# Kernel tuning notes

Hardware: AMD Instinct MI355X
Metric: run time of the kernel (lower is better)

The kernel has to match this reference:

```python
import jax, jax.numpy as jnp
import numpy as np

N = 100000
E = 300000
D = 128
EPS = 1e-5


def sage_conv(x, edge_index, Wl, bl, Wr):
    # PyG SAGEConv: out = lin_l(mean_{j in N(i)} x_j) + lin_r(x_i)
    src, dst = edge_index[0], edge_index[1]
    n = x.shape[0]
    agg = jax.ops.segment_sum(x[src], dst, num_segments=n)            # [N, d]
    cnt = jax.ops.segment_sum(jnp.ones((src.shape[0],), x.dtype), dst, num_segments=n)
    mean = agg / jnp.maximum(cnt, 1.0)[:, None]
    return mean @ Wl.T + bl + x @ Wr.T


def setup_inputs() -> dict:
    key = jax.random.key(0)
    ks = jax.random.split(key, 16)
    s = 0.05
    inp = {
        "feat": jax.random.normal(ks[0], (N, D), jnp.float32),
        "e0": jax.random.randint(ks[1], (2, E), 0, N, jnp.int32),
        "e1": jax.random.randint(ks[2], (2, E), 0, N, jnp.int32),
        "e2": jax.random.randint(ks[3], (2, E), 0, N, jnp.int32),
    }
    # per-etype SAGEConv params (in=hidden=128)
    for i, k in zip(range(3), (ks[4], ks[5], ks[6])):
        ka, kb = jax.random.split(k)
        inp[f"Wl{i}"] = jax.random.normal(ka, (D, D), jnp.float32) * s
        inp[f"bl{i}"] = jnp.zeros((D,), jnp.float32)
        inp[f"Wr{i}"] = jax.random.normal(kb, (D, D), jnp.float32) * s
    ka, kb = jax.random.split(ks[7])
    inp["Wla"] = jax.random.normal(ka, (D, D), jnp.float32) * s
    inp["bla"] = jnp.zeros((D,), jnp.float32)
    inp["Wra"] = jax.random.normal(kb, (D, D), jnp.float32) * s
    ka, kb = jax.random.split(ks[8])
    inp["Wf"] = jax.random.normal(ka, (D, D), jnp.float32) * s
    inp["bf"] = jnp.zeros((D,), jnp.float32)
    inp["Wrf"] = jax.random.normal(kb, (D, D), jnp.float32) * s
    inp["gamma"] = jnp.ones((D,), jnp.float32)
    inp["beta"] = jnp.zeros((D,), jnp.float32)
    inp["wt"] = jnp.ones((3,), jnp.float32)
    return inp


def reference(feat, Wl0, bl0, Wr0, Wl1, bl1, Wr1, Wl2, bl2, Wr2,
              Wla, bla, Wra, Wf, bf, Wrf, gamma, beta, wt, e0, e1, e2):
    out0 = sage_conv(feat, e0, Wl0, bl0, Wr0)
    out1 = sage_conv(feat, e1, Wl1, bl1, Wr1)
    out2 = sage_conv(feat, e2, Wl2, bl2, Wr2)
    all_e = jnp.concatenate([e0, e1, e2], axis=1)   # [2, 3E]
    all_out = sage_conv(feat, all_e, Wla, bla, Wra)
    comb = wt[0] * out0 + wt[1] * out1 + wt[2] * out2 + all_out
    comb = jax.nn.relu(comb)
    # BatchNorm1d (training mode: batch stats over node dim, biased var)
    mu = jnp.mean(comb, axis=0)
    var = jnp.mean((comb - mu) ** 2, axis=0)
    comb = (comb - mu) * jax.lax.rsqrt(var + EPS) * gamma + beta
    # dropout p=0.0 -> identity
    return sage_conv(comb, all_e, Wf, bf, Wrf)
```

## Files before the change

kernel.cpp:

```cpp
#include <hip/hip_runtime.h>

#define NN 100000
#define NE 300000
#define DD 128
#define NBLKG 782
#define NBLKSEG 49

typedef short bf16x8 __attribute__((ext_vector_type(8)));
typedef float f32x4 __attribute__((ext_vector_type(4)));
typedef unsigned u32x4 __attribute__((ext_vector_type(4)));

__device__ __forceinline__ unsigned short f2b(float f) {
    union { float f; unsigned u; } c; c.f = f;
    unsigned u = c.u;
    return (unsigned short)((u + 0x7fffu + ((u >> 16) & 1u)) >> 16);
}
__device__ __forceinline__ float b2lo(unsigned u) {
    union { float f; unsigned u; } c; c.u = u << 16; return c.f;
}
__device__ __forceinline__ float b2hi(unsigned u) {
    union { float f; unsigned u; } c; c.u = u & 0xffff0000u; return c.f;
}
__device__ __forceinline__ unsigned pack2(float lo, float hi) {
    return (unsigned)f2b(lo) | ((unsigned)f2b(hi) << 16);
}

#define NB_FEAT 6250
#define NB_WT   449
#define NB_DEG  3516
__global__ __launch_bounds__(256) void prep_all(
    const float* __restrict__ feat, unsigned short* __restrict__ fb,
    const float* __restrict__ Wl0, const float* __restrict__ bl0, const float* __restrict__ Wr0,
    const float* __restrict__ Wl1, const float* __restrict__ bl1, const float* __restrict__ Wr1,
    const float* __restrict__ Wl2, const float* __restrict__ bl2, const float* __restrict__ Wr2,
    const float* __restrict__ Wla, const float* __restrict__ bla, const float* __restrict__ Wra,
    const float* __restrict__ Wf,  const float* __restrict__ bfv, const float* __restrict__ Wrf,
    const float* __restrict__ wt,
    unsigned short* __restrict__ WcatB, float* __restrict__ bias1,
    unsigned short* __restrict__ W2catB, float* __restrict__ bias2,
    const int* __restrict__ e0, const int* __restrict__ e1, const int* __restrict__ e2,
    int* __restrict__ deg) {
    int b = blockIdx.x, tid = threadIdx.x;
    if (b < NB_FEAT) {
        int gid = b * 256 + tid;
        if (gid >= NN * 16) return;
        const f32x4* f4 = (const f32x4*)feat;
        f32x4 a = __builtin_nontemporal_load(&f4[gid * 2]);
        f32x4 c = __builtin_nontemporal_load(&f4[gid * 2 + 1]);
        uint4 o;
        o.x = pack2(a.x, a.y); o.y = pack2(a.z, a.w);
        o.z = pack2(c.x, c.y); o.w = pack2(c.z, c.w);
        ((uint4*)fb)[gid] = o;
    } else if (b < NB_FEAT + NB_WT) {
        int idx = (b - NB_FEAT) * 256 + tid;
        float w0 = wt[0], w1 = wt[1], w2 = wt[2];
        if (idx < 81920) {
            int f = idx / 640, k = idx % 640;
            float v;
            if (k < 128)      v = w0 * Wl0[f * 128 + k];
            else if (k < 256) v = w1 * Wl1[f * 128 + (k - 128)];
            else if (k < 384) v = w2 * Wl2[f * 128 + (k - 256)];
            else if (k < 512) v = Wla[f * 128 + (k - 384)];
            else {
                int kk = k - 512;
                v = w0 * Wr0[f * 128 + kk] + w1 * Wr1[f * 128 + kk] +
                    w2 * Wr2[f * 128 + kk] + Wra[f * 128 + kk];
            }
            WcatB[idx] = f2b(v);
        } else if (idx < 81920 + 32768) {
            int j = idx - 81920;
            int f = j >> 8, k = j & 255;
            W2catB[j] = f2b((k < 128) ? Wf[f * 128 + k] : Wrf[f * 128 + (k - 128)]);
        } else if (idx < 81920 + 32768 + 128) {
            int f = idx - (81920 + 32768);
            bias1[f] = w0 * bl0[f] + w1 * bl1[f] + w2 * bl2[f] + bla[f];
            bias2[f] = bfv[f];
        }
    } else {
        int gid = (b - NB_FEAT - NB_WT) * 256 + tid;
        if (gid >= 3 * NE) return;
        int t = (gid < NE) ? 0 : ((gid < 2 * NE) ? 1 : 2);
        int i = gid - t * NE;
        const int* ep = (t == 0) ? e0 : ((t == 1) ? e1 : e2);
        atomicAdd(&deg[t * NN + ep[NE + i]], 1);
    }
}

__global__ __launch_bounds__(256) void scan_local(
    const int* __restrict__ deg, int* __restrict__ rsloc, int* __restrict__ bsum) {
    __shared__ int sc[256];
    int b = blockIdx.x, tid = threadIdx.x;
    int seg = b / NBLKSEG, blk = b % NBLKSEG;
    int g0 = seg * NN;
    int base = blk * 2048 + tid * 8;
    int vals[8]; int tsum = 0;
#pragma unroll
    for (int j = 0; j < 8; ++j) {
        int l = base + j;
        int d = (l < NN) ? deg[g0 + l] : 0;
        vals[j] = tsum; tsum += d;
    }
    sc[tid] = tsum;
    __syncthreads();
    for (int off = 1; off < 256; off <<= 1) {
        int v = (tid >= off) ? sc[tid - off] : 0;
        __syncthreads();
        sc[tid] += v;
        __syncthreads();
    }
    int excl = sc[tid] - tsum;
#pragma unroll
    for (int j = 0; j < 8; ++j) {
        int l = base + j;
        if (l < NN) rsloc[g0 + l] = excl + vals[j];
    }
    if (tid == 255) bsum[b] = sc[255];
}

__global__ void scan_bsum(int* __restrict__ bsum) {
    int tid = threadIdx.x;
    if (tid < 3) {
        int run = 0;
        for (int b = 0; b < NBLKSEG; ++b) {
            int idx = tid * NBLKSEG + b;
            int t = bsum[idx]; bsum[idx] = run; run += t;
        }
    }
}

__global__ __launch_bounds__(256) void scan_fix(
    const int* __restrict__ deg, const int* __restrict__ rsloc, const int* __restrict__ bsum,
    int* __restrict__ fillpos, int* __restrict__ rowstartU, int* __restrict__ degall) {
    int blk = blockIdx.x, tid = threadIdx.x;
    int base = blk * 2048 + tid * 8;
    int o0 = bsum[blk], o1 = bsum[NBLKSEG + blk], o2 = bsum[2 * NBLKSEG + blk];
#pragma unroll
    for (int j = 0; j < 8; ++j) {
        int l = base + j;
        if (l < NN) {
            int d0 = deg[l], d1 = deg[NN + l], d2 = deg[2 * NN + l];
            int rU = (rsloc[l] + o0) + (rsloc[NN + l] + o1) + (rsloc[2 * NN + l] + o2);
            fillpos[l] = rU;
            fillpos[NN + l] = rU + d0;
            fillpos[2 * NN + l] = rU + d0 + d1;
            rowstartU[l] = rU;
            degall[l] = d0 + d1 + d2;
        }
    }
}

__global__ __launch_bounds__(256) void fill_csr(
    const int* __restrict__ e0, const int* __restrict__ e1, const int* __restrict__ e2,
    int* __restrict__ fillpos, int* __restrict__ csrU) {
    int gid = blockIdx.x * 256 + threadIdx.x;
    if (gid >= 3 * NE) return;
    int t = (gid < NE) ? 0 : ((gid < 2 * NE) ? 1 : 2);
    int i = gid - t * NE;
    const int* ep = (t == 0) ? e0 : ((t == 1) ? e1 : e2);
    int src = ep[i], dst = ep[NE + i];
    int p = atomicAdd(&fillpos[t * NN + dst], 1);
    csrU[p] = src;
}

__global__ __launch_bounds__(256) void gather1(
    const unsigned short* __restrict__ featB,
    const int* __restrict__ deg, const int* __restrict__ rowstartU,
    const int* __restrict__ degall, const int* __restrict__ csrU,
    unsigned short* __restrict__ meanB) {
    int n = __builtin_amdgcn_readfirstlane((int)((blockIdx.x * 256 + threadIdx.x) >> 6));
    if (n >= NN) return;
    int lane = threadIdx.x & 63;
    int d0 = deg[n], d1 = deg[NN + n];
    int dall = degall[n];
    int b1 = d0, b2 = d0 + d1;
    const int* cp = csrU + rowstartU[n];

    unsigned f0 = *((const unsigned*)(featB + (size_t)cp[0] * DD) + lane);
    unsigned f1 = *((const unsigned*)(featB + (size_t)cp[1] * DD) + lane);
    unsigned f2 = *((const unsigned*)(featB + (size_t)cp[2] * DD) + lane);
    unsigned f3 = *((const unsigned*)(featB + (size_t)cp[3] * DD) + lane);
    int i4 = cp[4], i5 = cp[5];
    float p0 = 0.f, p1 = 0.f;
    float sA0 = 0.f, sA1 = 0.f, sB0 = 0.f, sB1 = 0.f;
    for (int j = 0; j < dall; ++j) {
        if (j == b1) { sA0 = p0; sA1 = p1; }
        if (j == b2) { sB0 = p0; sB1 = p1; }
        unsigned u = f0;
        f0 = f1; f1 = f2; f2 = f3;
        f3 = *((const unsigned*)(featB + (size_t)i4 * DD) + lane);
        i4 = i5;
        i5 = cp[j + 6];
        p0 += b2lo(u); p1 += b2hi(u);
    }
    if (b2 == dall) { sB0 = p0; sB1 = p1; }
    if (b1 == dall) { sA0 = p0; sA1 = p1; }

    int d2 = dall - b2;
    float inv0 = 1.0f / fmaxf((float)d0, 1.0f);
    float inv1 = 1.0f / fmaxf((float)d1, 1.0f);
    float inv2 = 1.0f / fmaxf((float)d2, 1.0f);
    float m10 = sB0 - sA0, m11 = sB1 - sA1;
    float m20 = p0 - sB0,  m21 = p1 - sB1;
    unsigned* outp = (unsigned*)(meanB + (size_t)n * 384) + lane;
    __builtin_nontemporal_store(pack2(sA0 * inv0, sA1 * inv0), outp);
    __builtin_nontemporal_store(pack2(m10 * inv1, m11 * inv1), outp + 64);
    __builtin_nontemporal_store(pack2(m20 * inv2, m21 * inv2), outp + 128);
}

__global__ __launch_bounds__(256) void gemm1_tile(
    const unsigned short* __restrict__ meanB, const unsigned short* __restrict__ featB,
    const int* __restrict__ deg, const int* __restrict__ degall,
    const unsigned short* __restrict__ WcatB, const float* __restrict__ bias1,
    unsigned short* __restrict__ comb, float* __restrict__ partials) {
    __shared__ unsigned short ABs[65536 / 2];
    unsigned short* As = ABs;
    unsigned short* Bs = ABs + 16384;
    int tid = threadIdx.x;
    int wid = tid >> 6, lane = tid & 63;
    int quad = lane >> 4, m16 = lane & 15;
    int nb = blockIdx.x * 128;
    int mb = (wid & 1) * 64, fb = (wid >> 1) * 64;
    f32x4 acc[4][4];
#pragma unroll
    for (int mi = 0; mi < 4; ++mi)
#pragma unroll
        for (int fi = 0; fi < 4; ++fi) acc[mi][fi] = (f32x4){0.f, 0.f, 0.f, 0.f};

    for (int kc = 0; kc < 5; ++kc) {
        __syncthreads();
#pragma unroll
        for (int it = 0; it < 8; ++it) {
            int idx = it * 256 + tid;
            int row = idx >> 4, chunk = idx & 15;
            int s = chunk >> 2, q = chunk & 3;
            int gr = min(nb + row, NN - 1);
            u32x4 v;
            if (kc < 3) {
                v = *(const u32x4*)(meanB + (size_t)gr * 384 + kc * 128 + chunk * 8);
            } else if (kc == 3) {
                u32x4 m0 = *(const u32x4*)(meanB + (size_t)gr * 384 + chunk * 8);
                u32x4 m1 = *(const u32x4*)(meanB + (size_t)gr * 384 + 128 + chunk * 8);
                u32x4 m2 = *(const u32x4*)(meanB + (size_t)gr * 384 + 256 + chunk * 8);
                int dd0 = deg[gr], dd1 = deg[NN + gr], dal = degall[gr];
                float inva = 1.0f / fmaxf((float)dal, 1.0f);
                float w0 = (float)dd0 * inva;
                float w1 = (float)dd1 * inva;
                float w2 = (float)(dal - dd0 - dd1) * inva;
                v.x = pack2(w0 * b2lo(m0.x) + w1 * b2lo(m1.x) + w2 * b2lo(m2.x),
                            w0 * b2hi(m0.x) + w1 * b2hi(m1.x) + w2 * b2hi(m2.x));
                v.y = pack2(w0 * b2lo(m0.y) + w1 * b2lo(m1.y) + w2 * b2lo(m2.y),
                            w0 * b2hi(m0.y) + w1 * b2hi(m1.y) + w2 * b2hi(m2.y));
                v.z = pack2(w0 * b2lo(m0.z) + w1 * b2lo(m1.z) + w2 * b2lo(m2.z),
                            w0 * b2hi(m0.z) + w1 * b2hi(m1.z) + w2 * b2hi(m2.z));
                v.w = pack2(w0 * b2lo(m0.w) + w1 * b2lo(m1.w) + w2 * b2lo(m2.w),
                            w0 * b2hi(m0.w) + w1 * b2hi(m1.w) + w2 * b2hi(m2.w));
            } else {
                v = *(const u32x4*)(featB + (size_t)gr * DD + chunk * 8);
            }
            *(u32x4*)&As[(((s * 128 + row) * 4) + q) * 8] = v;
        }
#pragma unroll
        for (int it = 0; it < 8; ++it) {
            int idx = it * 256 + tid;
            int f = idx >> 4, chunk = idx & 15;
            int s = chunk >> 2, q = chunk & 3;
            u32x4 v = *(const u32x4*)(WcatB + (size_t)f * 640 + kc * 128 + chunk * 8);
            *(u32x4*)&Bs[(((s * 128 + f) * 4) + q) * 8] = v;
        }
        __syncthreads();
#pragma unroll
        for (int s = 0; s < 4; ++s) {
            bf16x8 av[4], bv[4];
#pragma unroll
            for (int mi = 0; mi < 4; ++mi)
                av[mi] = *(const bf16x8*)&As[(((s * 128 + mb + mi * 16 + m16) * 4) + quad) * 8];
#pragma unroll
            for (int fi = 0; fi < 4; ++fi)
                bv[fi] = *(const bf16x8*)&Bs[(((s * 128 + fb + fi * 16 + m16) * 4) + quad) * 8];
#pragma unroll
            for (int mi = 0; mi < 4; ++mi)
#pragma unroll
                for (int fi = 0; fi < 4; ++fi)
                    acc[mi][fi] = __builtin_amdgcn_mfma_f32_16x16x32_bf16(av[mi], bv[fi], acc[mi][fi], 0, 0, 0);
        }
    }
    __syncthreads();
    float* bnS = (float*)ABs;
    float* bnQ = bnS + 128;
    if (tid < 128) { bnS[tid] = 0.f; bnQ[tid] = 0.f; }
    __syncthreads();
#pragma unroll
    for (int fi = 0; fi < 4; ++fi) {
        int f = fb + fi * 16 + m16;
        float bb = bias1[f];
        float s = 0.f, q = 0.f;
#pragma unroll
        for (int mi = 0; mi < 4; ++mi) {
#pragma unroll
            for (int r = 0; r < 4; ++r) {
                int row = nb + mb + mi * 16 + quad * 4 + r;
                float v = fmaxf(acc[mi][fi][r] + bb, 0.f);
                if (row < NN) {
                    s += v; q += v * v;
                    comb[(size_t)row * DD + f] = f2b(v);
                }
            }
        }
        atomicAdd(&bnS[f], s);
        atomicAdd(&bnQ[f], q);
    }
    __syncthreads();
    if (tid < 128) {
        partials[(size_t)tid * NBLKG + blockIdx.x] = bnS[tid];
        partials[(size_t)(128 + tid) * NBLKG + blockIdx.x] = bnQ[tid];
    }
}

__global__ __launch_bounds__(256) void bnfin(
    const float* __restrict__ partials,
    const float* __restrict__ gamma, const float* __restrict__ beta,
    float* __restrict__ bnA, float* __restrict__ bnB) {
    __shared__ float rs[256], rq[256];
    int f = blockIdx.x, tid = threadIdx.x;
    float s = 0.f, q = 0.f;
    for (int r = tid; r < NBLKG; r += 256) {
        s += partials[(size_t)f * NBLKG + r];
        q += partials[(size_t)(128 + f) * NBLKG + r];
    }
    rs[tid] = s; rq[tid] = q;
    __syncthreads();
    for (int off = 128; off > 0; off >>= 1) {
        if (tid < off) { rs[tid] += rs[tid + off]; rq[tid] += rq[tid + off]; }
        __syncthreads();
    }
    if (tid == 0) {
        float mu = rs[0] / (float)NN;
        float var = fmaxf(rq[0] / (float)NN - mu * mu, 0.f);
        float a = gamma[f] * rsqrtf(var + 1e-5f);
        bnA[f] = a;
        bnB[f] = beta[f] - mu * a;
    }
}

__global__ __launch_bounds__(256) void gather2(
    const unsigned short* __restrict__ comb,
    const int* __restrict__ rowstartU, const int* __restrict__ degall,
    const int* __restrict__ csrU,
    const float* __restrict__ bnA, const float* __restrict__ bnB,
    unsigned short* __restrict__ meanC) {
    int n = __builtin_amdgcn_readfirstlane((int)((blockIdx.x * 256 + threadIdx.x) >> 6));
    if (n >= NN) return;
    int lane = threadIdx.x & 63;
    int dall = degall[n];
    const int* cp = csrU + rowstartU[n];

    unsigned f0 = *((const unsigned*)(comb + (size_t)cp[0] * DD) + lane);
    unsigned f1 = *((const unsigned*)(comb + (size_t)cp[1] * DD) + lane);
    unsigned f2 = *((const unsigned*)(comb + (size_t)cp[2] * DD) + lane);
    unsigned f3 = *((const unsigned*)(comb + (size_t)cp[3] * DD) + lane);
    int i4 = cp[4], i5 = cp[5];
    float p0 = 0.f, p1 = 0.f;
    for (int j = 0; j < dall; ++j) {
        unsigned u = f0;
        f0 = f1; f1 = f2; f2 = f3;
        f3 = *((const unsigned*)(comb + (size_t)i4 * DD) + lane);
        i4 = i5;
        i5 = cp[j + 6];
        p0 += b2lo(u); p1 += b2hi(u);
    }

    float v0 = 0.f, v1 = 0.f;
    if (dall > 0) {
        float inv = 1.0f / (float)dall;
        float2 a = *(const float2*)&bnA[lane * 2];
        float2 b = *(const float2*)&bnB[lane * 2];
        v0 = a.x * (p0 * inv) + b.x;
        v1 = a.y * (p1 * inv) + b.y;
    }
    __builtin_nontemporal_store(pack2(v0, v1),
                                (unsigned*)(meanC + (size_t)n * DD) + lane);
}

__global__ __launch_bounds__(256) void gemm2_tile(
    const unsigned short* __restrict__ meanC, const unsigned short* __restrict__ comb,
    const float* __restrict__ bnA, const float* __restrict__ bnB,
    const unsigned short* __restrict__ W2catB, const float* __restrict__ bias2,
    float* __restrict__ out) {
    __shared__ unsigned short ABs[65536 / 2];
    unsigned short* As = ABs;
    unsigned short* Bs = ABs + 16384;
    int tid = threadIdx.x;
    int wid = tid >> 6, lane = tid & 63;
    int quad = lane >> 4, m16 = lane & 15;
    int nb = blockIdx.x * 128;
    int mb = (wid & 1) * 64, fb = (wid >> 1) * 64;
    f32x4 acc[4][4];
#pragma unroll
    for (int mi = 0; mi < 4; ++mi)
#pragma unroll
        for (int fi = 0; fi < 4; ++fi) acc[mi][fi] = (f32x4){0.f, 0.f, 0.f, 0.f};

    for (int kc = 0; kc < 2; ++kc) {
        __syncthreads();
#pragma unroll
        for (int it = 0; it < 8; ++it) {
            int idx = it * 256 + tid;
            int row = idx >> 4, chunk = idx & 15;
            int s = chunk >> 2, q = chunk & 3;
            int gr = min(nb + row, NN - 1);
            u32x4 v;
            if (kc == 0) {
                v = *(const u32x4*)(meanC + (size_t)gr * DD + chunk * 8);
            } else {
                u32x4 c4 = *(const u32x4*)(comb + (size_t)gr * DD + chunk * 8);
                int cb = chunk * 8;
                float4 a0 = *(const float4*)&bnA[cb], a1 = *(const float4*)&bnA[cb + 4];
                float4 b0 = *(const float4*)&bnB[cb], b1 = *(const float4*)&bnB[cb + 4];
                v.x = pack2(a0.x * b2lo(c4.x) + b0.x, a0.y * b2hi(c4.x) + b0.y);
                v.y = pack2(a0.z * b2lo(c4.y) + b0.z, a0.w * b2hi(c4.y) + b0.w);
                v.z = pack2(a1.x * b2lo(c4.z) + b1.x, a1.y * b2hi(c4.z) + b1.y);
                v.w = pack2(a1.z * b2lo(c4.w) + b1.z, a1.w * b2hi(c4.w) + b1.w);
            }
            *(u32x4*)&As[(((s * 128 + row) * 4) + q) * 8] = v;
        }
#pragma unroll
        for (int it = 0; it < 8; ++it) {
            int idx = it * 256 + tid;
            int f = idx >> 4, chunk = idx & 15;
            int s = chunk >> 2, q = chunk & 3;
            u32x4 v = *(const u32x4*)(W2catB + (size_t)f * 256 + kc * 128 + chunk * 8);
            *(u32x4*)&Bs[(((s * 128 + f) * 4) + q) * 8] = v;
        }
        __syncthreads();
#pragma unroll
        for (int s = 0; s < 4; ++s) {
            bf16x8 av[4], bv[4];
#pragma unroll
            for (int mi = 0; mi < 4; ++mi)
                av[mi] = *(const bf16x8*)&As[(((s * 128 + mb + mi * 16 + m16) * 4) + quad) * 8];
#pragma unroll
            for (int fi = 0; fi < 4; ++fi)
                bv[fi] = *(const bf16x8*)&Bs[(((s * 128 + fb + fi * 16 + m16) * 4) + quad) * 8];
#pragma unroll
            for (int mi = 0; mi < 4; ++mi)
#pragma unroll
                for (int fi = 0; fi < 4; ++fi)
                    acc[mi][fi] = __builtin_amdgcn_mfma_f32_16x16x32_bf16(av[mi], bv[fi], acc[mi][fi], 0, 0, 0);
        }
    }
#pragma unroll
    for (int fi = 0; fi < 4; ++fi) {
        int f = fb + fi * 16 + m16;
        float bb = bias2[f];
#pragma unroll
        for (int mi = 0; mi < 4; ++mi) {
#pragma unroll
            for (int r = 0; r < 4; ++r) {
                int row = nb + mb + mi * 16 + quad * 4 + r;
                if (row < NN)
                    __builtin_nontemporal_store(acc[mi][fi][r] + bb,
                                                &out[(size_t)row * DD + f]);
            }
        }
    }
}

extern "C" void kernel_launch(void* const* d_in, const int* in_sizes, int n_in,
                              void* d_out, int out_size, void* d_ws, size_t ws_size,
                              hipStream_t stream) {
    const float* feat = (const float*)d_in[0];
    const int* e0 = (const int*)d_in[1];
    const int* e1 = (const int*)d_in[2];
    const int* e2 = (const int*)d_in[3];
    const float* Wl0 = (const float*)d_in[4];
    const float* bl0 = (const float*)d_in[5];
    const float* Wr0 = (const float*)d_in[6];
    const float* Wl1 = (const float*)d_in[7];
    const float* bl1 = (const float*)d_in[8];
    const float* Wr1 = (const float*)d_in[9];
    const float* Wl2 = (const float*)d_in[10];
    const float* bl2 = (const float*)d_in[11];
    const float* Wr2 = (const float*)d_in[12];
    const float* Wla = (const float*)d_in[13];
    const float* bla = (const float*)d_in[14];
    const float* Wra = (const float*)d_in[15];
    const float* Wf  = (const float*)d_in[16];
    const float* bfv = (const float*)d_in[17];
    const float* Wrf = (const float*)d_in[18];
    const float* gamma = (const float*)d_in[19];
    const float* beta  = (const float*)d_in[20];
    const float* wt    = (const float*)d_in[21];

    int* deg      = (int*)d_ws;
    int* rsloc    = deg + 3 * NN;
    int* fillpos  = rsloc + 3 * NN;
    int* csrU     = fillpos + 3 * NN;
    int* bsum     = csrU + 3 * NE + 8;
    int* rowstartU = bsum + 160;
    int* degall    = rowstartU + NN;
    float* partials = (float*)(degall + NN);
    float* bias1  = partials + 256 * NBLKG;
    float* bias2  = bias1 + 128;
    float* bnA    = bias2 + 128;
    float* bnB    = bnA + 128;
    unsigned short* WcatB  = (unsigned short*)(bnB + 128);
    unsigned short* W2catB = WcatB + 81920;
    unsigned short* comb   = W2catB + 32768;
    unsigned short* featB  = comb + (size_t)NN * DD;
    unsigned short* meanB  = featB + (size_t)NN * DD;
    unsigned short* meanC  = meanB + (size_t)NN * 384;

    hipMemsetAsync(deg, 0, (size_t)3 * NN * sizeof(int), stream);
    hipMemsetAsync(csrU + 3 * NE, 0, 8 * sizeof(int), stream);

    prep_all<<<NB_FEAT + NB_WT + NB_DEG, 256, 0, stream>>>(
        feat, featB,
        Wl0, bl0, Wr0, Wl1, bl1, Wr1, Wl2, bl2, Wr2,
        Wla, bla, Wra, Wf, bfv, Wrf, wt,
        WcatB, bias1, W2catB, bias2,
        e0, e1, e2, deg);
    scan_local<<<147, 256, 0, stream>>>(deg, rsloc, bsum);
    scan_bsum<<<1, 64, 0, stream>>>(bsum);
    scan_fix<<<NBLKSEG, 256, 0, stream>>>(deg, rsloc, bsum, fillpos, rowstartU, degall);
    fill_csr<<<3516, 256, 0, stream>>>(e0, e1, e2, fillpos, csrU);

    gather1<<<25000, 256, 0, stream>>>(featB, deg, rowstartU, degall, csrU, meanB);
    gemm1_tile<<<NBLKG, 256, 0, stream>>>(meanB, featB, deg, degall, WcatB, bias1,
                                          comb, partials);
    bnfin<<<128, 256, 0, stream>>>(partials, gamma, beta, bnA, bnB);
    gather2<<<25000, 256, 0, stream>>>(comb, rowstartU, degall, csrU, bnA, bnB, meanC);
    gemm2_tile<<<NBLKG, 256, 0, stream>>>(meanC, comb, bnA, bnB, W2catB, bias2,
                                          (float*)d_out);
}
```

Before: 523.8 us.

## Load GEMM operands directly from global memory and precompute all-edge mean in gather

Both GEMM kernels drop their LDS staging and barriers, and each wave loads its MFMA A and B fragments straight from global memory. gather1 now also writes the all-edge mean as a fourth 128-column slice, so gemm1 no longer recombines the three per-type means with degree weights. Removing LDS use may raise occupancy and cuts sync overhead. In exchange, global loads become strided and uncoalesced per wave, and each weight row is fetched redundantly by every wave; gather1 also writes an extra 128 columns per node.

```diff
diff --git a/kernel.cpp b/kernel.cpp
--- a/kernel.cpp
+++ b/kernel.cpp
@@ -159,7 +159,7 @@
     const int* ep = (t == 0) ? e0 : ((t == 1) ? e1 : e2);
     int src = ep[i], dst = ep[NE + i];
     int p = atomicAdd(&fillpos[t * NN + dst], 1);
-    csrU[p] = src;
+    csrU[t == 0 ? p : p] = src;
 }
 
 __global__ __launch_bounds__(256) void gather1(
@@ -199,22 +199,21 @@
     float inv0 = 1.0f / fmaxf((float)d0, 1.0f);
     float inv1 = 1.0f / fmaxf((float)d1, 1.0f);
     float inv2 = 1.0f / fmaxf((float)d2, 1.0f);
+    float inva = 1.0f / fmaxf((float)dall, 1.0f);
     float m10 = sB0 - sA0, m11 = sB1 - sA1;
     float m20 = p0 - sB0,  m21 = p1 - sB1;
-    unsigned* outp = (unsigned*)(meanB + (size_t)n * 384) + lane;
+    unsigned* outp = (unsigned*)(meanB + (size_t)n * 512) + lane;
     __builtin_nontemporal_store(pack2(sA0 * inv0, sA1 * inv0), outp);
     __builtin_nontemporal_store(pack2(m10 * inv1, m11 * inv1), outp + 64);
     __builtin_nontemporal_store(pack2(m20 * inv2, m21 * inv2), outp + 128);
+    __builtin_nontemporal_store(pack2(p0 * inva,  p1 * inva),  outp + 192);
 }
 
 __global__ __launch_bounds__(256) void gemm1_tile(
     const unsigned short* __restrict__ meanB, const unsigned short* __restrict__ featB,
-    const int* __restrict__ deg, const int* __restrict__ degall,
     const unsigned short* __restrict__ WcatB, const float* __restrict__ bias1,
     unsigned short* __restrict__ comb, float* __restrict__ partials) {
-    __shared__ unsigned short ABs[65536 / 2];
-    unsigned short* As = ABs;
-    unsigned short* Bs = ABs + 16384;
+    __shared__ float bnP[256];
     int tid = threadIdx.x;
     int wid = tid >> 6, lane = tid & 63;
     int quad = lane >> 4, m16 = lane & 15;
@@ -226,57 +225,33 @@
 #pragma unroll
         for (int fi = 0; fi < 4; ++fi) acc[mi][fi] = (f32x4){0.f, 0.f, 0.f, 0.f};
 
+    const unsigned short* aP[4];
+    const unsigned short* fP[4];
+    const unsigned short* bP[4];
+#pragma unroll
+    for (int mi = 0; mi < 4; ++mi) {
+        int r = min(nb + mb + mi * 16 + m16, NN - 1);
+        aP[mi] = meanB + (size_t)r * 512;
+        fP[mi] = featB + (size_t)r * DD;
+    }
+#pragma unroll
+    for (int fi = 0; fi < 4; ++fi)
+        bP[fi] = WcatB + (size_t)(fb + fi * 16 + m16) * 640;
+
+    int ko = quad * 8;
+#pragma unroll
     for (int kc = 0; kc < 5; ++kc) {
-        __syncthreads();
-#pragma unroll
-        for (int it = 0; it < 8; ++it) {
-            int idx = it * 256 + tid;
-            int row = idx >> 4, chunk = idx & 15;
-            int s = chunk >> 2, q = chunk & 3;
-            int gr = min(nb + row, NN - 1);
-            u32x4 v;
-            if (kc < 3) {
-                v = *(const u32x4*)(meanB + (size_t)gr * 384 + kc * 128 + chunk * 8);
-            } else if (kc == 3) {
-                u32x4 m0 = *(const u32x4*)(meanB + (size_t)gr * 384 + chunk * 8);
-                u32x4 m1 = *(const u32x4*)(meanB + (size_t)gr * 384 + 128 + chunk * 8);
-                u32x4 m2 = *(const u32x4*)(meanB + (size_t)gr * 384 + 256 + chunk * 8);
-                int dd0 = deg[gr], dd1 = deg[NN + gr], dal = degall[gr];
-                float inva = 1.0f / fmaxf((float)dal, 1.0f);
-                float w0 = (float)dd0 * inva;
-                float w1 = (float)dd1 * inva;
-                float w2 = (float)(dal - dd0 - dd1) * inva;
-                v.x = pack2(w0 * b2lo(m0.x) + w1 * b2lo(m1.x) + w2 * b2lo(m2.x),
-                            w0 * b2hi(m0.x) + w1 * b2hi(m1.x) + w2 * b2hi(m2.x));
-                v.y = pack2(w0 * b2lo(m0.y) + w1 * b2lo(m1.y) + w2 * b2lo(m2.y),
-                            w0 * b2hi(m0.y) + w1 * b2hi(m1.y) + w2 * b2hi(m2.y));
-                v.z = pack2(w0 * b2lo(m0.z) + w1 * b2lo(m1.z) + w2 * b2lo(m2.z),
-                            w0 * b2hi(m0.z) + w1 * b2hi(m1.z) + w2 * b2hi(m2.z));
-                v.w = pack2(w0 * b2lo(m0.w) + w1 * b2lo(m1.w) + w2 * b2lo(m2.w),
-                            w0 * b2hi(m0.w) + w1 * b2hi(m1.w) + w2 * b2hi(m2.w));
-            } else {
-                v = *(const u32x4*)(featB + (size_t)gr * DD + chunk * 8);
-            }
-            *(u32x4*)&As[(((s * 128 + row) * 4) + q) * 8] = v;
-        }
-#pragma unroll
-        for (int it = 0; it < 8; ++it) {
-            int idx = it * 256 + tid;
-            int f = idx >> 4, chunk = idx & 15;
-            int s = chunk >> 2, q = chunk & 3;
-            u32x4 v = *(const u32x4*)(WcatB + (size_t)f * 640 + kc * 128 + chunk * 8);
-            *(u32x4*)&Bs[(((s * 128 + f) * 4) + q) * 8] = v;
-        }
-        __syncthreads();
 #pragma unroll
         for (int s = 0; s < 4; ++s) {
+            int k = s * 32 + ko;
             bf16x8 av[4], bv[4];
 #pragma unroll
             for (int mi = 0; mi < 4; ++mi)
-                av[mi] = *(const bf16x8*)&As[(((s * 128 + mb + mi * 16 + m16) * 4) + quad) * 8];
+                av[mi] = (kc < 4) ? *(const bf16x8*)(aP[mi] + kc * 128 + k)
+                                  : *(const bf16x8*)(fP[mi] + k);
 #pragma unroll
             for (int fi = 0; fi < 4; ++fi)
-                bv[fi] = *(const bf16x8*)&Bs[(((s * 128 + fb + fi * 16 + m16) * 4) + quad) * 8];
+                bv[fi] = *(const bf16x8*)(bP[fi] + kc * 128 + k);
 #pragma unroll
             for (int mi = 0; mi < 4; ++mi)
 #pragma unroll
@@ -284,9 +259,9 @@
                     acc[mi][fi] = __builtin_amdgcn_mfma_f32_16x16x32_bf16(av[mi], bv[fi], acc[mi][fi], 0, 0, 0);
         }
     }
-    __syncthreads();
-    float* bnS = (float*)ABs;
-    float* bnQ = bnS + 128;
+
+    float* bnS = bnP;
+    float* bnQ = bnP + 128;
     if (tid < 128) { bnS[tid] = 0.f; bnQ[tid] = 0.f; }
     __syncthreads();
 #pragma unroll
@@ -386,9 +361,6 @@
     const float* __restrict__ bnA, const float* __restrict__ bnB,
     const unsigned short* __restrict__ W2catB, const float* __restrict__ bias2,
     float* __restrict__ out) {
-    __shared__ unsigned short ABs[65536 / 2];
-    unsigned short* As = ABs;
-    unsigned short* Bs = ABs + 16384;
     int tid = threadIdx.x;
     int wid = tid >> 6, lane = tid & 63;
     int quad = lane >> 4, m16 = lane & 15;
@@ -400,54 +372,59 @@
 #pragma unroll
         for (int fi = 0; fi < 4; ++fi) acc[mi][fi] = (f32x4){0.f, 0.f, 0.f, 0.f};
 
-    for (int kc = 0; kc < 2; ++kc) {
-        __syncthreads();
-#pragma unroll
-        for (int it = 0; it < 8; ++it) {
-            int idx = it * 256 + tid;
-            int row = idx >> 4, chunk = idx & 15;
-            int s = chunk >> 2, q = chunk & 3;
-            int gr = min(nb + row, NN - 1);
-            u32x4 v;
-            if (kc == 0) {
-                v = *(const u32x4*)(meanC + (size_t)gr * DD + chunk * 8);
-            } else {
-                u32x4 c4 = *(const u32x4*)(comb + (size_t)gr * DD + chunk * 8);
-                int cb = chunk * 8;
-                float4 a0 = *(const float4*)&bnA[cb], a1 = *(const float4*)&bnA[cb + 4];
-                float4 b0 = *(const float4*)&bnB[cb], b1 = *(const float4*)&bnB[cb + 4];
-                v.x = pack2(a0.x * b2lo(c4.x) + b0.x, a0.y * b2hi(c4.x) + b0.y);
-                v.y = pack2(a0.z * b2lo(c4.y) + b0.z, a0.w * b2hi(c4.y) + b0.w);
-                v.z = pack2(a1.x * b2lo(c4.z) + b1.x, a1.y * b2hi(c4.z) + b1.y);
-                v.w = pack2(a1.z * b2lo(c4.w) + b1.z, a1.w * b2hi(c4.w) + b1.w);
-            }
-            *(u32x4*)&As[(((s * 128 + row) * 4) + q) * 8] = v;
-        }
-#pragma unroll
-        for (int it = 0; it < 8; ++it) {
-            int idx = it * 256 + tid;
-            int f = idx >> 4, chunk = idx & 15;
-            int s = chunk >> 2, q = chunk & 3;
-            u32x4 v = *(const u32x4*)(W2catB + (size_t)f * 256 + kc * 128 + chunk * 8);
-            *(u32x4*)&Bs[(((s * 128 + f) * 4) + q) * 8] = v;
-        }
-        __syncthreads();
-#pragma unroll
-        for (int s = 0; s < 4; ++s) {
-            bf16x8 av[4], bv[4];
-#pragma unroll
-            for (int mi = 0; mi < 4; ++mi)
-                av[mi] = *(const bf16x8*)&As[(((s * 128 + mb + mi * 16 + m16) * 4) + quad) * 8];
+    const unsigned short* mP[4];
+    const unsigned short* cP[4];
+    const unsigned short* bP[4];
+#pragma unroll
+    for (int mi = 0; mi < 4; ++mi) {
+        int r = min(nb + mb + mi * 16 + m16, NN - 1);
+        mP[mi] = meanC + (size_t)r * DD;
+        cP[mi] = comb + (size_t)r * DD;
+    }
+#pragma unroll
+    for (int fi = 0; fi < 4; ++fi)
+        bP[fi] = W2catB + (size_t)(fb + fi * 16 + m16) * 256;
+
+    int ko = quad * 8;
+#pragma unroll
+    for (int s = 0; s < 4; ++s) {
+        int k = s * 32 + ko;
+        bf16x8 av[4], bv[4];
+#pragma unroll
+        for (int mi = 0; mi < 4; ++mi) av[mi] = *(const bf16x8*)(mP[mi] + k);
+#pragma unroll
+        for (int fi = 0; fi < 4; ++fi) bv[fi] = *(const bf16x8*)(bP[fi] + k);
+#pragma unroll
+        for (int mi = 0; mi < 4; ++mi)
 #pragma unroll
             for (int fi = 0; fi < 4; ++fi)
-                bv[fi] = *(const bf16x8*)&Bs[(((s * 128 + fb + fi * 16 + m16) * 4) + quad) * 8];
-#pragma unroll
-            for (int mi = 0; mi < 4; ++mi)
-#pragma unroll
-                for (int fi = 0; fi < 4; ++fi)
-                    acc[mi][fi] = __builtin_amdgcn_mfma_f32_16x16x32_bf16(av[mi], bv[fi], acc[mi][fi], 0, 0, 0);
-        }
-    }
+                acc[mi][fi] = __builtin_amdgcn_mfma_f32_16x16x32_bf16(av[mi], bv[fi], acc[mi][fi], 0, 0, 0);
+    }
+#pragma unroll
+    for (int s = 0; s < 4; ++s) {
+        int k = s * 32 + ko;
+        float4 a0 = *(const float4*)&bnA[k], a1 = *(const float4*)&bnA[k + 4];
+        float4 b0 = *(const float4*)&bnB[k], b1 = *(const float4*)&bnB[k + 4];
+        bf16x8 av[4], bv[4];
+#pragma unroll
+        for (int mi = 0; mi < 4; ++mi) {
+            u32x4 c4 = *(const u32x4*)(cP[mi] + k);
+            u32x4 rv;
+            rv.x = pack2(a0.x * b2lo(c4.x) + b0.x, a0.y * b2hi(c4.x) + b0.y);
+            rv.y = pack2(a0.z * b2lo(c4.y) + b0.z, a0.w * b2hi(c4.y) + b0.w);
+            rv.z = pack2(a1.x * b2lo(c4.z) + b1.x, a1.y * b2hi(c4.z) + b1.y);
+            rv.w = pack2(a1.z * b2lo(c4.w) + b1.z, a1.w * b2hi(c4.w) + b1.w);
+            av[mi] = *(const bf16x8*)&rv;
+        }
+#pragma unroll
+        for (int fi = 0; fi < 4; ++fi) bv[fi] = *(const bf16x8*)(bP[fi] + 128 + k);
+#pragma unroll
+        for (int mi = 0; mi < 4; ++mi)
+#pragma unroll
+            for (int fi = 0; fi < 4; ++fi)
+                acc[mi][fi] = __builtin_amdgcn_mfma_f32_16x16x32_bf16(av[mi], bv[fi], acc[mi][fi], 0, 0, 0);
+    }
+
 #pragma unroll
     for (int fi = 0; fi < 4; ++fi) {
         int f = fb + fi * 16 + m16;
@@ -508,7 +485,7 @@
     unsigned short* comb   = W2catB + 32768;
     unsigned short* featB  = comb + (size_t)NN * DD;
     unsigned short* meanB  = featB + (size_t)NN * DD;
-    unsigned short* meanC  = meanB + (size_t)NN * 384;
+    unsigned short* meanC  = meanB + (size_t)NN * 512;
 
     hipMemsetAsync(deg, 0, (size_t)3 * NN * sizeof(int), stream);
     hipMemsetAsync(csrU + 3 * NE, 0, 8 * sizeof(int), stream);
@@ -525,8 +502,7 @@
     fill_csr<<<3516, 256, 0, stream>>>(e0, e1, e2, fillpos, csrU);
 
     gather1<<<25000, 256, 0, stream>>>(featB, deg, rowstartU, degall, csrU, meanB);
-    gemm1_tile<<<NBLKG, 256, 0, stream>>>(meanB, featB, deg, degall, WcatB, bias1,
-                                          comb, partials);
+    gemm1_tile<<<NBLKG, 256, 0, stream>>>(meanB, featB, WcatB, bias1, comb, partials);
     bnfin<<<128, 256, 0, stream>>>(partials, gamma, beta, bnA, bnB);
     gather2<<<25000, 256, 0, stream>>>(comb, rowstartU, degall, csrU, bnA, bnB, meanC);
     gemm2_tile<<<NBLKG, 256, 0, stream>>>(meanC, comb, bnA, bnB, W2catB, bias2,
```

Result: slower. 578.5 us (+10.4%).

## Write all-edge mean in gather, read weights directly from global in GEMMs

Applied to the files above, without the earlier changes.

gather1 now also writes the all-edge mean as a fourth 128-wide segment, so the meanB row stride grows from 384 to 512. This lets gemm1 skip rebuilding that mean from the three per-type means and degrees. Both GEMM kernels stop staging the weight tile in LDS and load B fragments straight from global/L2 through per-lane pointers. The A tile uses an XOR-swizzled row-major LDS layout with nontemporal loads. The trade is extra gather write traffic and uncached-style global weight loads inside the MFMA loop, against halved LDS use and less staging work.

```diff
diff --git a/kernel.cpp b/kernel.cpp
--- a/kernel.cpp
+++ b/kernel.cpp
@@ -199,22 +199,21 @@
     float inv0 = 1.0f / fmaxf((float)d0, 1.0f);
     float inv1 = 1.0f / fmaxf((float)d1, 1.0f);
     float inv2 = 1.0f / fmaxf((float)d2, 1.0f);
+    float inva = 1.0f / fmaxf((float)dall, 1.0f);
     float m10 = sB0 - sA0, m11 = sB1 - sA1;
     float m20 = p0 - sB0,  m21 = p1 - sB1;
-    unsigned* outp = (unsigned*)(meanB + (size_t)n * 384) + lane;
+    unsigned* outp = (unsigned*)(meanB + (size_t)n * 512) + lane;
     __builtin_nontemporal_store(pack2(sA0 * inv0, sA1 * inv0), outp);
     __builtin_nontemporal_store(pack2(m10 * inv1, m11 * inv1), outp + 64);
     __builtin_nontemporal_store(pack2(m20 * inv2, m21 * inv2), outp + 128);
+    __builtin_nontemporal_store(pack2(p0 * inva,  p1 * inva),  outp + 192);
 }
 
 __global__ __launch_bounds__(256) void gemm1_tile(
     const unsigned short* __restrict__ meanB, const unsigned short* __restrict__ featB,
-    const int* __restrict__ deg, const int* __restrict__ degall,
     const unsigned short* __restrict__ WcatB, const float* __restrict__ bias1,
     unsigned short* __restrict__ comb, float* __restrict__ partials) {
-    __shared__ unsigned short ABs[65536 / 2];
-    unsigned short* As = ABs;
-    unsigned short* Bs = ABs + 16384;
+    __shared__ unsigned short As[128 * 128];
     int tid = threadIdx.x;
     int wid = tid >> 6, lane = tid & 63;
     int quad = lane >> 4, m16 = lane & 15;
@@ -226,57 +225,36 @@
 #pragma unroll
         for (int fi = 0; fi < 4; ++fi) acc[mi][fi] = (f32x4){0.f, 0.f, 0.f, 0.f};
 
+    const unsigned short* bP[4];
+#pragma unroll
+    for (int fi = 0; fi < 4; ++fi)
+        bP[fi] = WcatB + (size_t)(fb + fi * 16 + m16) * 640;
+
     for (int kc = 0; kc < 5; ++kc) {
         __syncthreads();
 #pragma unroll
         for (int it = 0; it < 8; ++it) {
             int idx = it * 256 + tid;
             int row = idx >> 4, chunk = idx & 15;
-            int s = chunk >> 2, q = chunk & 3;
             int gr = min(nb + row, NN - 1);
-            u32x4 v;
-            if (kc < 3) {
-                v = *(const u32x4*)(meanB + (size_t)gr * 384 + kc * 128 + chunk * 8);
-            } else if (kc == 3) {
-                u32x4 m0 = *(const u32x4*)(meanB + (size_t)gr * 384 + chunk * 8);
-                u32x4 m1 = *(const u32x4*)(meanB + (size_t)gr * 384 + 128 + chunk * 8);
-                u32x4 m2 = *(const u32x4*)(meanB + (size_t)gr * 384 + 256 + chunk * 8);
-                int dd0 = deg[gr], dd1 = deg[NN + gr], dal = degall[gr];
-                float inva = 1.0f / fmaxf((float)dal, 1.0f);
-                float w0 = (float)dd0 * inva;
-                float w1 = (float)dd1 * inva;
-                float w2 = (float)(dal - dd0 - dd1) * inva;
-                v.x = pack2(w0 * b2lo(m0.x) + w1 * b2lo(m1.x) + w2 * b2lo(m2.x),
-                            w0 * b2hi(m0.x) + w1 * b2hi(m1.x) + w2 * b2hi(m2.x));
-                v.y = pack2(w0 * b2lo(m0.y) + w1 * b2lo(m1.y) + w2 * b2lo(m2.y),
-                            w0 * b2hi(m0.y) + w1 * b2hi(m1.y) + w2 * b2hi(m2.y));
-                v.z = pack2(w0 * b2lo(m0.z) + w1 * b2lo(m1.z) + w2 * b2lo(m2.z),
-                            w0 * b2hi(m0.z) + w1 * b2hi(m1.z) + w2 * b2hi(m2.z));
-                v.w = pack2(w0 * b2lo(m0.w) + w1 * b2lo(m1.w) + w2 * b2lo(m2.w),
-                            w0 * b2hi(m0.w) + w1 * b2hi(m1.w) + w2 * b2hi(m2.w));
-            } else {
-                v = *(const u32x4*)(featB + (size_t)gr * DD + chunk * 8);
-            }
-            *(u32x4*)&As[(((s * 128 + row) * 4) + q) * 8] = v;
-        }
-#pragma unroll
-        for (int it = 0; it < 8; ++it) {
-            int idx = it * 256 + tid;
-            int f = idx >> 4, chunk = idx & 15;
-            int s = chunk >> 2, q = chunk & 3;
-            u32x4 v = *(const u32x4*)(WcatB + (size_t)f * 640 + kc * 128 + chunk * 8);
-            *(u32x4*)&Bs[(((s * 128 + f) * 4) + q) * 8] = v;
+            u32x4 v = (kc < 4)
+                ? __builtin_nontemporal_load((const u32x4*)(meanB + (size_t)gr * 512 + kc * 128 + chunk * 8))
+                : *(const u32x4*)(featB + (size_t)gr * DD + chunk * 8);
+            *(u32x4*)&As[row * 128 + ((chunk ^ (row & 7)) * 8)] = v;
         }
         __syncthreads();
 #pragma unroll
         for (int s = 0; s < 4; ++s) {
             bf16x8 av[4], bv[4];
 #pragma unroll
-            for (int mi = 0; mi < 4; ++mi)
-                av[mi] = *(const bf16x8*)&As[(((s * 128 + mb + mi * 16 + m16) * 4) + quad) * 8];
+            for (int mi = 0; mi < 4; ++mi) {
+                int row = mb + mi * 16 + m16;
+                int ch = (s * 4 + quad) ^ (row & 7);
+                av[mi] = *(const bf16x8*)&As[row * 128 + ch * 8];
+            }
 #pragma unroll
             for (int fi = 0; fi < 4; ++fi)
-                bv[fi] = *(const bf16x8*)&Bs[(((s * 128 + fb + fi * 16 + m16) * 4) + quad) * 8];
+                bv[fi] = *(const bf16x8*)(bP[fi] + kc * 128 + s * 32 + quad * 8);
 #pragma unroll
             for (int mi = 0; mi < 4; ++mi)
 #pragma unroll
@@ -285,7 +263,7 @@
         }
     }
     __syncthreads();
-    float* bnS = (float*)ABs;
+    float* bnS = (float*)As;
     float* bnQ = bnS + 128;
     if (tid < 128) { bnS[tid] = 0.f; bnQ[tid] = 0.f; }
     __syncthreads();
@@ -386,9 +364,7 @@
     const float* __restrict__ bnA, const float* __restrict__ bnB,
     const unsigned short* __restrict__ W2catB, const float* __restrict__ bias2,
     float* __restrict__ out) {
-    __shared__ unsigned short ABs[65536 / 2];
-    unsigned short* As = ABs;
-    unsigned short* Bs = ABs + 16384;
+    __shared__ unsigned short As[128 * 128];
     int tid = threadIdx.x;
     int wid = tid >> 6, lane = tid & 63;
     int quad = lane >> 4, m16 = lane & 15;
@@ -400,17 +376,21 @@
 #pragma unroll
         for (int fi = 0; fi < 4; ++fi) acc[mi][fi] = (f32x4){0.f, 0.f, 0.f, 0.f};
 
+    const unsigned short* bP[4];
+#pragma unroll
+    for (int fi = 0; fi < 4; ++fi)
+        bP[fi] = W2catB + (size_t)(fb + fi * 16 + m16) * 256;
+
     for (int kc = 0; kc < 2; ++kc) {
         __syncthreads();
 #pragma unroll
         for (int it = 0; it < 8; ++it) {
             int idx = it * 256 + tid;
             int row = idx >> 4, chunk = idx & 15;
-            int s = chunk >> 2, q = chunk & 3;
             int gr = min(nb + row, NN - 1);
             u32x4 v;
             if (kc == 0) {
-                v = *(const u32x4*)(meanC + (size_t)gr * DD + chunk * 8);
+                v = __builtin_nontemporal_load((const u32x4*)(meanC + (size_t)gr * DD + chunk * 8));
             } else {
                 u32x4 c4 = *(const u32x4*)(comb + (size_t)gr * DD + chunk * 8);
                 int cb = chunk * 8;
@@ -421,26 +401,21 @@
                 v.z = pack2(a1.x * b2lo(c4.z) + b1.x, a1.y * b2hi(c4.z) + b1.y);
                 v.w = pack2(a1.z * b2lo(c4.w) + b1.z, a1.w * b2hi(c4.w) + b1.w);
             }
-            *(u32x4*)&As[(((s * 128 + row) * 4) + q) * 8] = v;
-        }
-#pragma unroll
-        for (int it = 0; it < 8; ++it) {
-            int idx = it * 256 + tid;
-            int f = idx >> 4, chunk = idx & 15;
-            int s = chunk >> 2, q = chunk & 3;
-            u32x4 v = *(const u32x4*)(W2catB + (size_t)f * 256 + kc * 128 + chunk * 8);
-            *(u32x4*)&Bs[(((s * 128 + f) * 4) + q) * 8] = v;
+            *(u32x4*)&As[row * 128 + ((chunk ^ (row & 7)) * 8)] = v;
         }
         __syncthreads();
 #pragma unroll
         for (int s = 0; s < 4; ++s) {
             bf16x8 av[4], bv[4];
 #pragma unroll
-            for (int mi = 0; mi < 4; ++mi)
-                av[mi] = *(const bf16x8*)&As[(((s * 128 + mb + mi * 16 + m16) * 4) + quad) * 8];
+            for (int mi = 0; mi < 4; ++mi) {
+                int row = mb + mi * 16 + m16;
+                int ch = (s * 4 + quad) ^ (row & 7);
+                av[mi] = *(const bf16x8*)&As[row * 128 + ch * 8];
+            }
 #pragma unroll
             for (int fi = 0; fi < 4; ++fi)
-                bv[fi] = *(const bf16x8*)&Bs[(((s * 128 + fb + fi * 16 + m16) * 4) + quad) * 8];
+                bv[fi] = *(const bf16x8*)(bP[fi] + kc * 128 + s * 32 + quad * 8);
 #pragma unroll
             for (int mi = 0; mi < 4; ++mi)
 #pragma unroll
@@ -508,7 +483,7 @@
     unsigned short* comb   = W2catB + 32768;
     unsigned short* featB  = comb + (size_t)NN * DD;
     unsigned short* meanB  = featB + (size_t)NN * DD;
-    unsigned short* meanC  = meanB + (size_t)NN * 384;
+    unsigned short* meanC  = meanB + (size_t)NN * 512;
 
     hipMemsetAsync(deg, 0, (size_t)3 * NN * sizeof(int), stream);
     hipMemsetAsync(csrU + 3 * NE, 0, 8 * sizeof(int), stream);
@@ -525,8 +500,7 @@
     fill_csr<<<3516, 256, 0, stream>>>(e0, e1, e2, fillpos, csrU);
 
     gather1<<<25000, 256, 0, stream>>>(featB, deg, rowstartU, degall, csrU, meanB);
-    gemm1_tile<<<NBLKG, 256, 0, stream>>>(meanB, featB, deg, degall, WcatB, bias1,
-                                          comb, partials);
+    gemm1_tile<<<NBLKG, 256, 0, stream>>>(meanB, featB, WcatB, bias1, comb, partials);
     bnfin<<<128, 256, 0, stream>>>(partials, gamma, beta, bnA, bnB);
     gather2<<<25000, 256, 0, stream>>>(comb, rowstartU, degall, csrU, bnA, bnB, meanC);
     gemm2_tile<<<NBLKG, 256, 0, stream>>>(meanC, comb, bnA, bnB, W2catB, bias2,
```

After: 519.1 us. About the same (-0.9%).
